# Performance work log

Measured on AMD Instinct MI355X. Metric: run time of the kernel, lower is better.

The kernel has to match this reference:

```python
import jax, jax.numpy as jnp
import numpy as np

BLOCK = 7          # hardcoded block_size
NUM_HEADS = 32     # CLIP RN50 attnpool heads
OUT_DIM = 512      # attnpool output dim == text feature dim
VOTE_CH = 512      # hardcoded channel count of `result`
NUM_BUCKETS = 6
_BOUNDS = jnp.array([8, 15, 22, 29, 36])  # class-index -> bucket boundaries from the if/elif chain


def _forward(image_features, text_features, pos_embed, q_w, q_b, k_w, k_b, v_w, v_b, out_w, out_b):
    B, C, Hf, Wf = image_features.shape
    Ho, Wo = Hf - BLOCK + 1, Wf - BLOCK + 1
    dt = image_features.dtype
    # --- batched extraction of all 7x7 sliding windows (replaces the i,j Python loop) ---
    ii = jnp.arange(Ho)[:, None] + jnp.arange(BLOCK)   # [Ho,7]
    jj = jnp.arange(Wo)[:, None] + jnp.arange(BLOCK)   # [Wo,7]
    rows = image_features[:, :, ii, :]                 # [B,C,Ho,7,Wf]
    pat = rows[:, :, :, :, jj]                         # [B,C,Ho,7,Wo,7]
    # row-major (di,dj) token order matches x.flatten(2) in CLIP AttentionPool2d
    tokens = pat.transpose(0, 2, 4, 3, 5, 1).reshape(B, Ho * Wo, BLOCK * BLOCK, C)  # [B,P,49,C]
    # --- CLIP AttentionPool2d, batched over all windows ---
    x = jnp.concatenate([tokens.mean(axis=2, keepdims=True), tokens], axis=2) + pos_embed  # [B,P,50,C]
    P, T = x.shape[1], x.shape[2]
    hd = C // NUM_HEADS
    q = (x[:, :, :1] @ q_w.T + q_b).reshape(B, P, 1, NUM_HEADS, hd)   # query = mean token
    k = (x @ k_w.T + k_b).reshape(B, P, T, NUM_HEADS, hd)
    v = (x @ v_w.T + v_b).reshape(B, P, T, NUM_HEADS, hd)
    attn = jax.nn.softmax(jnp.einsum('bpqhd,bpkhd->bphqk', q, k) * (float(hd) ** -0.5), axis=-1)
    pooled = jnp.einsum('bphqk,bpkhd->bpqhd', attn, v).reshape(B, P, C) @ out_w.T + out_b  # [B,P,512]
    # F.normalize followed by an extra /= norm (idempotent, kept for faithfulness)
    f = pooled / jnp.maximum(jnp.linalg.norm(pooled, axis=-1, keepdims=True), 1e-12)
    f = f / jnp.linalg.norm(f, axis=-1, keepdims=True)
    txt = text_features / jnp.linalg.norm(text_features, axis=-1, keepdims=True)
    logits = 100.0 * (f @ txt.T)                        # softmax is monotone -> argmax(logits)==argmax(probs)
    idx = jnp.argmax(logits, axis=-1)                   # [B,P]
    bucket = jnp.searchsorted(_BOUNDS, idx, side='right')  # 6-way grouping per the if/elif chain
    onehot = jax.nn.one_hot(bucket, NUM_BUCKETS, dtype=dt).reshape(B, Ho, Wo, NUM_BUCKETS).transpose(0, 3, 1, 2)
    # vote scatter-add (+1 over each 7x7 window) == full cross-correlation with a ones kernel
    kern = jnp.ones((NUM_BUCKETS, 1, BLOCK, BLOCK), dt)
    votes = jax.lax.conv_general_dilated(onehot, kern, (1, 1), [(BLOCK - 1, BLOCK - 1)] * 2,
                                         dimension_numbers=('NCHW', 'OIHW', 'NCHW'),
                                         feature_group_count=NUM_BUCKETS)  # [B,6,Hf,Wf]
    max_idx = jnp.argmax(votes, axis=1).astype(dt)      # torch.max returns first max index; argmax matches
    # `result` is re-created inside the per-image loop, so only slot B-1 survives (faithful to original)
    result = jnp.zeros((B, VOTE_CH, Hf, Wf), dt).at[B - 1].set(
        jnp.broadcast_to(max_idx[B - 1][None], (VOTE_CH, Hf, Wf)))
    return result / jnp.maximum(jnp.linalg.norm(result, axis=1, keepdims=True), 1e-12)


def setup_inputs() -> dict:
    key = jax.random.key(0)
    ks = jax.random.split(key, 8)
    B, C, Hf, Wf, NT = 2, 2048, 24, 24, 45
    w = lambda k, s: jax.random.normal(k, s, jnp.float32) * 0.02
    return {
        'image_features': jax.random.normal(ks[0], (B, C, Hf, Wf), jnp.float32),
        'text_features': jax.random.normal(ks[1], (NT, OUT_DIM), jnp.float32),
        'pos_embed': w(ks[2], (BLOCK * BLOCK + 1, C)),
        'q_w': w(ks[3], (C, C)), 'q_b': jnp.zeros((C,), jnp.float32),
        'k_w': w(ks[4], (C, C)), 'k_b': jnp.zeros((C,), jnp.float32),
        'v_w': w(ks[5], (C, C)), 'v_b': jnp.zeros((C,), jnp.float32),
        'out_w': w(ks[6], (OUT_DIM, C)), 'out_b': jnp.zeros((OUT_DIM,), jnp.float32),
    }


def reference(image_features, text_features, pos_embed, q_w, q_b, k_w, k_b, v_w, v_b, out_w, out_b):
    return _forward(image_features, text_features, pos_embed, q_w, q_b, k_w, k_b, v_w, v_b, out_w, out_b)
```

## Files before the change

kernel.cpp:

```cpp
#include <hip/hip_runtime.h>
#include <math.h>

#define CDIM 2048
#define HF 24
#define WF 24
#define PIX 576
#define HO 18
#define WO 18
#define NP 324
#define NHEAD 32
#define HD 64
#define NTOK 50
#define NTXT 45
#define OUTD 512
#define NKV 626
#define HJ (NHEAD * NTXT)
#define NROWS 640

typedef __attribute__((ext_vector_type(8))) short short8;
typedef __attribute__((ext_vector_type(4))) float f32x4;
typedef __attribute__((address_space(1))) const void as1c_void;
typedef __attribute__((address_space(3))) void as3_void;

__device__ inline unsigned bf16rn(float x) {
    unsigned u = __float_as_uint(x);
    return (u + 0x7FFFu + ((u >> 16) & 1u)) >> 16;
}
__device__ inline float bf16tof(unsigned h) { return __uint_as_float(h << 16); }

__device__ inline size_t frag_off(int row, int k) {
    return (size_t)(((row >> 4) * 64 + (k >> 5)) * 512)
         + (size_t)(((k & 31) >> 3) * 128 + (row & 15) * 8 + (k & 7));
}

__global__ void split_w_k(const float* __restrict__ kw, const float* __restrict__ vw, const float* __restrict__ qw,
                          ushort* __restrict__ WhK, ushort* __restrict__ WlK,
                          ushort* __restrict__ WhV, ushort* __restrict__ WlV,
                          ushort* __restrict__ WhQ, ushort* __restrict__ WlQ) {
    int g = blockIdx.x * 256 + threadIdx.x;
    int sel = g >> 20;
    int off = (g & 1048575) * 4;
    const float* src = sel == 0 ? kw : sel == 1 ? vw : qw;
    ushort* dh = sel == 0 ? WhK : sel == 1 ? WhV : WhQ;
    ushort* dl = sel == 0 ? WlK : sel == 1 ? WlV : WlQ;
    float4 v = *(const float4*)(src + off);
    float xs[4] = {v.x, v.y, v.z, v.w};
    ushort h[4], l[4];
#pragma unroll
    for (int i = 0; i < 4; ++i) {
        unsigned hh = bf16rn(xs[i]);
        h[i] = (ushort)hh;
        l[i] = (ushort)bf16rn(xs[i] - bf16tof(hh));
    }
    int m = off >> 11, k0 = off & 2047;
    size_t fo = frag_off(m, k0);
    *(ushort4*)(dh + fo) = make_ushort4(h[0], h[1], h[2], h[3]);
    *(ushort4*)(dl + fo) = make_ushort4(l[0], l[1], l[2], l[3]);
}

__global__ __launch_bounds__(256) void split_xt_k(const float* __restrict__ feat1,
                                                  ushort* __restrict__ Xh, ushort* __restrict__ Xl) {
    __shared__ float tile[64][65];
    int n0 = blockIdx.x * 64, c0 = blockIdx.y * 64, tid = threadIdx.x;
#pragma unroll
    for (int i = 0; i < 16; ++i) {
        int idx = tid + i * 256;
        int cc = idx >> 6, nn = idx & 63;
        tile[cc][nn] = feat1[(size_t)(c0 + cc) * PIX + n0 + nn];
    }
    __syncthreads();
#pragma unroll
    for (int i = 0; i < 16; ++i) {
        int idx = tid + i * 256;
        int nn = idx >> 6, cc = idx & 63;
        float x = tile[cc][nn];
        unsigned hh = bf16rn(x);
        size_t fo = frag_off(n0 + nn, c0 + cc);
        Xh[fo] = (ushort)hh;
        Xl[fo] = (ushort)bf16rn(x - bf16tof(hh));
    }
}

__global__ void split_pos_k(const float* __restrict__ pos,
                            ushort* __restrict__ Xh, ushort* __restrict__ Xl) {
    int g = blockIdx.x * 256 + threadIdx.x;
    int r = g >> 9;
    int c = (g & 511) * 4;
    float4 v = make_float4(0.f, 0.f, 0.f, 0.f);
    if (r < 50) v = *(const float4*)(pos + (size_t)r * CDIM + c);
    float xs[4] = {v.x, v.y, v.z, v.w};
    ushort h[4], l[4];
#pragma unroll
    for (int i = 0; i < 4; ++i) {
        unsigned hh = bf16rn(xs[i]);
        h[i] = (ushort)hh;
        l[i] = (ushort)bf16rn(xs[i] - bf16tof(hh));
    }
    size_t fo = frag_off(576 + r, c);
    *(ushort4*)(Xh + fo) = make_ushort4(h[0], h[1], h[2], h[3]);
    *(ushort4*)(Xl + fo) = make_ushort4(l[0], l[1], l[2], l[3]);
}

#define BUFB 24576
__global__ __launch_bounds__(256, 2) void gemm_bf16_k(
    const ushort* __restrict__ WhK, const ushort* __restrict__ WlK,
    const ushort* __restrict__ WhV, const ushort* __restrict__ WlV,
    const ushort* __restrict__ WhQ, const ushort* __restrict__ WlQ,
    const ushort* __restrict__ Xh, const ushort* __restrict__ Xl,
    const float* __restrict__ k_b, const float* __restrict__ v_b, const float* __restrict__ q_b,
    float* __restrict__ Kbuf, float* __restrict__ Vbuf, float* __restrict__ Qfull)
{
    __shared__ char smem[3 * BUFB];
    int z = blockIdx.z;
    const ushort* Wh = z == 0 ? WhK : z == 1 ? WhV : WhQ;
    const ushort* Wl = z == 0 ? WlK : z == 1 ? WlV : WlQ;
    const float* bias = z == 0 ? k_b : z == 1 ? v_b : q_b;
    float* out = z == 0 ? Kbuf : z == 1 ? Vbuf : Qfull;
    int m0 = blockIdx.x * 128, n0 = blockIdx.y * 64;

    int tid = threadIdx.x, wid = tid >> 6, lane = tid & 63;
    int wm = wid >> 1, wn = wid & 1;

    const char* gsrc[6];
    int ldsoff[6];
#pragma unroll
    for (int i = 0; i < 6; ++i) {
        int g = wid * 6 + i;
        const ushort* src; int r16; int off;
        if (g < 8)       { src = Wh; r16 = (m0 >> 4) + g;        off = g * 1024; }
        else if (g < 16) { src = Wl; r16 = (m0 >> 4) + (g - 8);  off = 8192 + (g - 8) * 1024; }
        else if (g < 20) { src = Xh; r16 = (n0 >> 4) + (g - 16); off = 16384 + (g - 16) * 1024; }
        else             { src = Xl; r16 = (n0 >> 4) + (g - 20); off = 20480 + (g - 20) * 1024; }
        gsrc[i] = (const char*)src + ((size_t)r16 * 64 * 1024) + lane * 16;
        ldsoff[i] = off;
    }

    f32x4 acc[4][2];
#pragma unroll
    for (int a = 0; a < 4; ++a)
#pragma unroll
        for (int b = 0; b < 2; ++b) acc[a][b] = (f32x4)0.f;

#pragma unroll
    for (int i = 0; i < 6; ++i)
        __builtin_amdgcn_global_load_lds((as1c_void*)(gsrc[i]),
                                         (as3_void*)(smem + ldsoff[i]), 16, 0, 0);
#pragma unroll
    for (int i = 0; i < 6; ++i)
        __builtin_amdgcn_global_load_lds((as1c_void*)(gsrc[i] + 1024),
                                         (as3_void*)(smem + BUFB + ldsoff[i]), 16, 0, 0);
    asm volatile("s_waitcnt vmcnt(6)" ::: "memory");
    __builtin_amdgcn_s_barrier();
    asm volatile("" ::: "memory");

    for (int t = 0; t < 64; ++t) {
        char* rbuf = smem + (t % 3) * BUFB;
        if (t < 62) {
            char* wbuf = smem + ((t + 2) % 3) * BUFB;
#pragma unroll
            for (int i = 0; i < 6; ++i)
                __builtin_amdgcn_global_load_lds((as1c_void*)(gsrc[i] + (size_t)(t + 2) * 1024),
                                                 (as3_void*)(wbuf + ldsoff[i]), 16, 0, 0);
        }

        short8 ah[4], al[4];
#pragma unroll
        for (int fm = 0; fm < 4; ++fm) {
            int s = wm * 4 + fm;
            ah[fm] = *(const short8*)(rbuf + s * 1024 + lane * 16);
            al[fm] = *(const short8*)(rbuf + 8192 + s * 1024 + lane * 16);
        }
        short8 bh[2], bl[2];
#pragma unroll
        for (int fn = 0; fn < 2; ++fn) {
            int s = wn * 2 + fn;
            bh[fn] = *(const short8*)(rbuf + 16384 + s * 1024 + lane * 16);
            bl[fn] = *(const short8*)(rbuf + 20480 + s * 1024 + lane * 16);
        }
#pragma unroll
        for (int fn = 0; fn < 2; ++fn)
#pragma unroll
            for (int fm = 0; fm < 4; ++fm) {
                acc[fm][fn] = __builtin_amdgcn_mfma_f32_16x16x32_bf16(ah[fm], bh[fn], acc[fm][fn], 0, 0, 0);
                acc[fm][fn] = __builtin_amdgcn_mfma_f32_16x16x32_bf16(ah[fm], bl[fn], acc[fm][fn], 0, 0, 0);
                acc[fm][fn] = __builtin_amdgcn_mfma_f32_16x16x32_bf16(al[fm], bh[fn], acc[fm][fn], 0, 0, 0);
            }

        if (t < 62) asm volatile("s_waitcnt vmcnt(6)" ::: "memory");
        else        asm volatile("s_waitcnt vmcnt(0)" ::: "memory");
        __builtin_amdgcn_s_barrier();
        asm volatile("" ::: "memory");
    }

#pragma unroll
    for (int fm = 0; fm < 4; ++fm) {
        int mg = m0 + wm * 64 + fm * 16 + (lane >> 4) * 4;
        float4 bv = *(const float4*)(bias + mg);
#pragma unroll
        for (int fn = 0; fn < 2; ++fn) {
            int ng = n0 + wn * 32 + fn * 16 + (lane & 15);
            f32x4 o = acc[fm][fn];
            if (ng >= PIX) { o[0] += bv.x; o[1] += bv.y; o[2] += bv.z; o[3] += bv.w; }
            *(f32x4*)(out + (size_t)ng * CDIM + mg) = o;
        }
    }
}

__global__ __launch_bounds__(256) void qmean_k(const float* __restrict__ Qfull, float* __restrict__ Qm) {
    int p = blockIdx.x;
    int i = p / WO, j = p % WO;
    int c = blockIdx.y * 1024 + threadIdx.x * 4;
    float4 s = make_float4(0.f, 0.f, 0.f, 0.f);
#pragma unroll 7
    for (int t = 0; t < 49; ++t) {
        int px = (i + t / 7) * WF + (j + t % 7);
        float4 v = *(const float4*)(Qfull + (size_t)px * CDIM + c);
        s.x += v.x; s.y += v.y; s.z += v.z; s.w += v.w;
    }
    float4 p0 = *(const float4*)(Qfull + (size_t)PIX * CDIM + c);
    float4 r;
    r.x = s.x * (1.f / 49.f) + p0.x;
    r.y = s.y * (1.f / 49.f) + p0.y;
    r.z = s.z * (1.f / 49.f) + p0.z;
    r.w = s.w * (1.f / 49.f) + p0.w;
    *(float4*)(Qm + (size_t)p * CDIM + c) = r;
}

__global__ __launch_bounds__(256) void txtw_k(
    const float* __restrict__ txt, const float* __restrict__ out_w, const float* __restrict__ out_b,
    float* __restrict__ TW, float* __restrict__ cconst)
{
    __shared__ float ts[OUTD];
    __shared__ float red[256], redb[256];
    int j = blockIdx.x, cb = blockIdx.y, tid = threadIdx.x;

    float n2 = 0.f, db = 0.f;
    for (int o = tid; o < OUTD; o += 256) {
        float tv = txt[(size_t)j * OUTD + o];
        ts[o] = tv;
        n2 += tv * tv;
        db += tv * out_b[o];
    }
    red[tid] = n2; redb[tid] = db;
    __syncthreads();
    for (int s = 128; s > 0; s >>= 1) {
        if (tid < s) { red[tid] += red[tid + s]; redb[tid] += redb[tid + s]; }
        __syncthreads();
    }
    float inv = 1.f / sqrtf(red[0]);

    int c = cb * 256 + tid;
    float acc = 0.f;
    for (int o = 0; o < OUTD; ++o)
        acc += ts[o] * out_w[(size_t)o * CDIM + c];
    TW[(size_t)j * CDIM + c] = acc * inv;
    if (cb == 0 && tid == 0) cconst[j] = redb[0] * inv;
}

__global__ __launch_bounds__(256) void tv_k(
    const float* __restrict__ TW, const float* __restrict__ Vbuf, float* __restrict__ TV)
{
    __shared__ float TWs[NTXT * HD];
    __shared__ float Vs[8 * HD];
    int cg = blockIdx.x, h = blockIdx.y, tid = threadIdx.x;
    int c0 = cg * 8;

    for (int idx = tid; idx < NTXT * HD; idx += 256) {
        int j = idx / HD, d = idx % HD;
        TWs[idx] = TW[(size_t)j * CDIM + h * HD + d];
    }
    for (int idx = tid; idx < 8 * HD; idx += 256) {
        int c = idx / HD, d = idx % HD;
        int col = c0 + c;
        Vs[idx] = (col < NKV) ? Vbuf[(size_t)col * CDIM + h * HD + d] : 0.f;
    }
    __syncthreads();

    for (int o = tid; o < 8 * NTXT; o += 256) {
        int c = o / NTXT, j = o % NTXT;
        int col = c0 + c;
        if (col >= NKV) continue;
        float acc = 0.f;
#pragma unroll
        for (int d = 0; d < HD; d += 4) {
            float4 tw = *(const float4*)&TWs[j * HD + d];
            float4 vv = *(const float4*)&Vs[c * HD + d];
            acc += tw.x * vv.x + tw.y * vv.y + tw.z * vv.z + tw.w * vv.w;
        }
        TV[(size_t)col * HJ + h * NTXT + j] = acc;
    }
}

__global__ __launch_bounds__(384) void attn_fused_k(
    const float* __restrict__ Kbuf, const float* __restrict__ Qm,
    const float* __restrict__ TV, float* __restrict__ pooledHJ)
{
    __shared__ float qs[8 * HD];
    __shared__ float scf[8][NTOK];
    __shared__ float scp[8][NTOK];
    __shared__ int win[49];

    int p = blockIdx.x, s = blockIdx.y;
    int h0 = s * 8;
    int pi = p / WO, pj = p % WO;
    int tid = threadIdx.x;

    if (tid < 128)
        *(float4*)&qs[tid * 4] = *(const float4*)(Qm + (size_t)p * CDIM + h0 * HD + tid * 4);
    if (tid < 49)
        win[tid] = (pi + tid / 7) * WF + (pj + tid % 7);
    __syncthreads();

    int grp = tid >> 4, gl = tid & 15;
#pragma unroll 3
    for (int i = 0; i < 33; ++i) {
        int pair = grp * 33 + i;
        int h, tt, row;
        if (pair < 392) { h = pair / 49; tt = pair % 49; row = win[tt]; }
        else { int q = pair - 392; h = q / 50; tt = q % 50; row = PIX + tt; }
        float4 kv = *(const float4*)(Kbuf + (size_t)row * CDIM + (h0 + h) * HD + gl * 4);
        float4 qv = *(const float4*)&qs[h * HD + gl * 4];
        float d = kv.x * qv.x + kv.y * qv.y + kv.z * qv.z + kv.w * qv.w;
        d += __shfl_xor(d, 1);
        d += __shfl_xor(d, 2);
        d += __shfl_xor(d, 4);
        d += __shfl_xor(d, 8);
        if (gl == 0) {
            if (pair < 392) scf[h][tt + 1] = d;
            else            scp[h][tt] = d;
        }
    }
    __syncthreads();

    if (tid < 8) {
        int h = tid;
        float sF = 0.f;
        for (int t = 1; t < NTOK; ++t) sF += scf[h][t];
        scf[h][0] = sF * (1.f / 49.f);
        float m = -1e30f;
        for (int t = 0; t < NTOK; ++t) {
            float sc = (scf[h][t] + scp[h][t]) * 0.125f;
            scp[h][t] = sc;
            m = fmaxf(m, sc);
        }
        float ssum = 0.f;
        for (int t = 0; t < NTOK; ++t) { float e = expf(scp[h][t] - m); scf[h][t] = e; ssum += e; }
        float inv = 1.f / ssum;
        for (int t = 0; t < NTOK; ++t) scf[h][t] *= inv;
    }
    __syncthreads();

    if (tid < 360) {
        int o = s * 360 + tid;
        int hloc = tid / 45;
        const float* apr = &scf[hloc][0];
        float lacc = 0.f, macc = 0.f;
#pragma unroll 7
        for (int t = 1; t < NTOK; ++t) {
            float a = apr[t];
            float v1 = TV[(size_t)win[t - 1] * HJ + o];
            float v2 = TV[(size_t)(PIX + t) * HJ + o];
            lacc += a * (v1 + v2);
            macc += v1;
        }
        float a0 = apr[0];
        lacc += a0 * (macc * (1.f / 49.f) + TV[(size_t)PIX * HJ + o]);
        pooledHJ[(size_t)p * HJ + o] = lacc;
    }
}

__global__ __launch_bounds__(64) void finish_k(const float* __restrict__ pooledHJ,
                                               const float* __restrict__ cconst,
                                               int* __restrict__ bucket) {
    __shared__ float lg[NTXT];
    int p = blockIdx.x, lane = threadIdx.x;
    if (lane < NTXT) {
        float s = cconst[lane];
        const float* row = pooledHJ + (size_t)p * HJ;
#pragma unroll 8
        for (int h = 0; h < NHEAD; ++h) s += row[h * NTXT + lane];
        lg[lane] = s;
    }
    __syncthreads();
    if (lane == 0) {
        float best = lg[0]; int bi = 0;
        for (int j2 = 1; j2 < NTXT; ++j2)
            if (lg[j2] > best) { best = lg[j2]; bi = j2; }
        int bk = 0;
        const int bounds[5] = {8, 15, 22, 29, 36};
#pragma unroll
        for (int u = 0; u < 5; ++u) bk += (bi >= bounds[u]) ? 1 : 0;
        bucket[p] = bk;
    }
}

__global__ void votes_k(const int* __restrict__ bucket, float* __restrict__ maxval) {
    __shared__ int bk[NP];
    int tid = threadIdx.x;
    if (tid < NP) bk[tid] = bucket[tid];
    __syncthreads();
    if (tid < PIX) {
        int y = tid / WF, x = tid % WF;
        int cnt[6] = {0, 0, 0, 0, 0, 0};
        int i0 = (y - 6 < 0) ? 0 : y - 6;
        int i1 = (y > HO - 1) ? HO - 1 : y;
        int j0 = (x - 6 < 0) ? 0 : x - 6;
        int j1 = (x > WO - 1) ? WO - 1 : x;
        for (int i = i0; i <= i1; ++i)
            for (int j = j0; j <= j1; ++j)
                cnt[bk[i * WO + j]]++;
        int best = cnt[0], bi = 0;
#pragma unroll
        for (int ch = 1; ch < 6; ++ch)
            if (cnt[ch] > best) { best = cnt[ch]; bi = ch; }
        maxval[tid] = (bi > 0) ? 0.044194173824159216f : 0.f;
    }
}

__global__ void fill_k(const float* __restrict__ maxval, float* __restrict__ out) {
    int idx = blockIdx.x * 256 + threadIdx.x;
    const int HALF = OUTD * PIX;
    if (idx >= 2 * HALF) return;
    out[idx] = (idx < HALF) ? 0.f : maxval[idx % PIX];
}

extern "C" void kernel_launch(void* const* d_in, const int* in_sizes, int n_in,
                              void* d_out, int out_size, void* d_ws, size_t ws_size,
                              hipStream_t stream) {
    const float* imgf = (const float*)d_in[0];
    const float* txt  = (const float*)d_in[1];
    const float* pos  = (const float*)d_in[2];
    const float* q_w  = (const float*)d_in[3];
    const float* q_b  = (const float*)d_in[4];
    const float* k_w  = (const float*)d_in[5];
    const float* k_b  = (const float*)d_in[6];
    const float* v_w  = (const float*)d_in[7];
    const float* v_b  = (const float*)d_in[8];
    const float* o_w  = (const float*)d_in[9];
    const float* o_b  = (const float*)d_in[10];

    const float* feat1 = imgf + (size_t)1 * CDIM * PIX;

    float* ws = (float*)d_ws;
    float* Kbuf  = ws;
    float* Vbuf  = Kbuf + (size_t)NROWS * CDIM;
    float* Qfull = Vbuf + (size_t)NROWS * CDIM;
    float* Qm    = Qfull + (size_t)NROWS * CDIM;
    float* TW    = Qm + (size_t)NP * CDIM;
    float* cconst = TW + (size_t)NTXT * CDIM;
    float* TV    = cconst + 64;
    float* pooledHJ = TV + (size_t)NKV * HJ;
    int*   bucket = (int*)(pooledHJ + (size_t)NP * HJ);
    float* maxval = (float*)(bucket + NP);
    size_t foff = (size_t)(maxval + 576 - ws);
    foff = (foff + 3) & ~(size_t)3;
    ushort* WhK = (ushort*)(ws + foff);
    ushort* WlK = WhK + (size_t)CDIM * CDIM;
    ushort* WhV = WlK + (size_t)CDIM * CDIM;
    ushort* WlV = WhV + (size_t)CDIM * CDIM;
    ushort* WhQ = WlV + (size_t)CDIM * CDIM;
    ushort* WlQ = WhQ + (size_t)CDIM * CDIM;
    ushort* Xh  = WlQ + (size_t)CDIM * CDIM;
    ushort* Xl  = Xh + (size_t)NROWS * CDIM;

    split_w_k<<<dim3(12288), dim3(256), 0, stream>>>(k_w, v_w, q_w, WhK, WlK, WhV, WlV, WhQ, WlQ);
    split_xt_k<<<dim3(9, 32), dim3(256), 0, stream>>>(feat1, Xh, Xl);
    split_pos_k<<<dim3(128), dim3(256), 0, stream>>>(pos, Xh, Xl);
    gemm_bf16_k<<<dim3(16, 10, 3), dim3(256), 0, stream>>>(WhK, WlK, WhV, WlV, WhQ, WlQ,
                                                           Xh, Xl, k_b, v_b, q_b, Kbuf, Vbuf, Qfull);
    qmean_k<<<dim3(NP, 2), dim3(256), 0, stream>>>(Qfull, Qm);
    txtw_k<<<dim3(NTXT, 8), dim3(256), 0, stream>>>(txt, o_w, o_b, TW, cconst);
    tv_k<<<dim3(79, 32), dim3(256), 0, stream>>>(TW, Vbuf, TV);
    attn_fused_k<<<dim3(NP, 4), dim3(384), 0, stream>>>(Kbuf, Qm, TV, pooledHJ);
    finish_k<<<dim3(NP), dim3(64), 0, stream>>>(pooledHJ, cconst, bucket);
    votes_k<<<dim3(1), dim3(576), 0, stream>>>(bucket, maxval);
    fill_k<<<dim3(2304), dim3(256), 0, stream>>>(maxval, (float*)d_out);
}
```

Before: 234.9 us.

## Precompute pos-embedding key scores in separate kernel and parallelize attention softmax

Moves the query·positional-key dot products into a new poss_k kernel that writes a per-window score table, which attn_fused_k then loads instead of computing them. The fused kernel's loop over key pairs shrinks to the 392 window tokens, and the per-head softmax is spread across 16 lanes per head with shuffle reductions instead of 8 serial threads. The grid is also flattened and remapped so neighbouring blocks cover adjacent windows and head groups, which may improve cache reuse. The cost is an extra kernel launch and an extra global buffer round trip.

```diff
diff --git a/kernel.cpp b/kernel.cpp
--- a/kernel.cpp
+++ b/kernel.cpp
@@ -226,6 +226,27 @@
     *(float4*)(Qm + (size_t)p * CDIM + c) = r;
 }
 
+__global__ __launch_bounds__(256) void poss_k(const float* __restrict__ Kbuf,
+                                              const float* __restrict__ Qm,
+                                              float* __restrict__ POSS) {
+    __shared__ float qsl[4 * HD];
+    int pb = blockIdx.x * 4, h = blockIdx.y, tid = threadIdx.x;
+    qsl[tid] = Qm[(size_t)(pb + (tid >> 6)) * CDIM + h * HD + (tid & 63)];
+    __syncthreads();
+    if (tid < 200) {
+        int pp = tid / 50, t = tid % 50;
+        const float* kp = Kbuf + (size_t)(PIX + t) * CDIM + h * HD;
+        const float* q = &qsl[pp * HD];
+        float dot = 0.f;
+#pragma unroll
+        for (int d = 0; d < HD; d += 4) {
+            float4 kv = *(const float4*)&kp[d];
+            dot += kv.x * q[d] + kv.y * q[d + 1] + kv.z * q[d + 2] + kv.w * q[d + 3];
+        }
+        POSS[(size_t)(pb + pp) * (NHEAD * NTOK) + h * NTOK + t] = dot;
+    }
+}
+
 __global__ __launch_bounds__(256) void txtw_k(
     const float* __restrict__ txt, const float* __restrict__ out_w, const float* __restrict__ out_b,
     float* __restrict__ TW, float* __restrict__ cconst)
@@ -293,14 +314,17 @@
 
 __global__ __launch_bounds__(384) void attn_fused_k(
     const float* __restrict__ Kbuf, const float* __restrict__ Qm,
-    const float* __restrict__ TV, float* __restrict__ pooledHJ)
+    const float* __restrict__ TV, const float* __restrict__ POSS,
+    float* __restrict__ pooledHJ)
 {
     __shared__ float qs[8 * HD];
     __shared__ float scf[8][NTOK];
     __shared__ float scp[8][NTOK];
     __shared__ int win[49];
 
-    int p = blockIdx.x, s = blockIdx.y;
+    int flat = blockIdx.x;
+    int s = (flat & 7) >> 1;
+    int p = (flat >> 3) * 2 + (flat & 1);
     int h0 = s * 8;
     int pi = p / WO, pj = p % WO;
     int tid = threadIdx.x;
@@ -309,44 +333,68 @@
         *(float4*)&qs[tid * 4] = *(const float4*)(Qm + (size_t)p * CDIM + h0 * HD + tid * 4);
     if (tid < 49)
         win[tid] = (pi + tid / 7) * WF + (pj + tid % 7);
+    for (int u = tid; u < 8 * NTOK; u += 384)
+        scp[u / NTOK][u % NTOK] = POSS[(size_t)p * (NHEAD * NTOK) + h0 * NTOK + u];
     __syncthreads();
 
     int grp = tid >> 4, gl = tid & 15;
-#pragma unroll 3
-    for (int i = 0; i < 33; ++i) {
-        int pair = grp * 33 + i;
-        int h, tt, row;
-        if (pair < 392) { h = pair / 49; tt = pair % 49; row = win[tt]; }
-        else { int q = pair - 392; h = q / 50; tt = q % 50; row = PIX + tt; }
-        float4 kv = *(const float4*)(Kbuf + (size_t)row * CDIM + (h0 + h) * HD + gl * 4);
-        float4 qv = *(const float4*)&qs[h * HD + gl * 4];
-        float d = kv.x * qv.x + kv.y * qv.y + kv.z * qv.z + kv.w * qv.w;
-        d += __shfl_xor(d, 1);
-        d += __shfl_xor(d, 2);
-        d += __shfl_xor(d, 4);
-        d += __shfl_xor(d, 8);
-        if (gl == 0) {
-            if (pair < 392) scf[h][tt + 1] = d;
-            else            scp[h][tt] = d;
-        }
-    }
-    __syncthreads();
-
-    if (tid < 8) {
-        int h = tid;
-        float sF = 0.f;
-        for (int t = 1; t < NTOK; ++t) sF += scf[h][t];
-        scf[h][0] = sF * (1.f / 49.f);
-        float m = -1e30f;
-        for (int t = 0; t < NTOK; ++t) {
-            float sc = (scf[h][t] + scp[h][t]) * 0.125f;
-            scp[h][t] = sc;
-            m = fmaxf(m, sc);
-        }
-        float ssum = 0.f;
-        for (int t = 0; t < NTOK; ++t) { float e = expf(scp[h][t] - m); scf[h][t] = e; ssum += e; }
-        float inv = 1.f / ssum;
-        for (int t = 0; t < NTOK; ++t) scf[h][t] *= inv;
+    for (int i = 0; i < 17; ++i) {
+        int pair = i * 24 + grp;
+        if (pair < 392) {
+            int h = pair / 49, tt = pair % 49;
+            float4 kv = *(const float4*)(Kbuf + (size_t)win[tt] * CDIM + (h0 + h) * HD + gl * 4);
+            float4 qv = *(const float4*)&qs[h * HD + gl * 4];
+            float d = kv.x * qv.x + kv.y * qv.y + kv.z * qv.z + kv.w * qv.w;
+            d += __shfl_xor(d, 1);
+            d += __shfl_xor(d, 2);
+            d += __shfl_xor(d, 4);
+            d += __shfl_xor(d, 8);
+            if (gl == 0) scf[h][tt + 1] = d;
+        }
+    }
+    __syncthreads();
+
+    if (tid < 128) {
+        int h = grp;
+        float sloc = 0.f;
+#pragma unroll
+        for (int i = 0; i < 4; ++i) {
+            int t = gl + 16 * i;
+            if (t >= 1 && t < NTOK) sloc += scf[h][t];
+        }
+        sloc += __shfl_xor(sloc, 1); sloc += __shfl_xor(sloc, 2);
+        sloc += __shfl_xor(sloc, 4); sloc += __shfl_xor(sloc, 8);
+        float s0 = sloc * (1.f / 49.f);
+
+        float sc[4];
+        float mloc = -1e30f;
+#pragma unroll
+        for (int i = 0; i < 4; ++i) {
+            int t = gl + 16 * i;
+            if (t < NTOK) {
+                float base = (t == 0) ? s0 : scf[h][t];
+                sc[i] = (base + scp[h][t]) * 0.125f;
+                mloc = fmaxf(mloc, sc[i]);
+            }
+        }
+        mloc = fmaxf(mloc, __shfl_xor(mloc, 1)); mloc = fmaxf(mloc, __shfl_xor(mloc, 2));
+        mloc = fmaxf(mloc, __shfl_xor(mloc, 4)); mloc = fmaxf(mloc, __shfl_xor(mloc, 8));
+
+        float ev[4];
+        float eloc = 0.f;
+#pragma unroll
+        for (int i = 0; i < 4; ++i) {
+            int t = gl + 16 * i;
+            if (t < NTOK) { ev[i] = expf(sc[i] - mloc); eloc += ev[i]; }
+        }
+        eloc += __shfl_xor(eloc, 1); eloc += __shfl_xor(eloc, 2);
+        eloc += __shfl_xor(eloc, 4); eloc += __shfl_xor(eloc, 8);
+        float inv = 1.f / eloc;
+#pragma unroll
+        for (int i = 0; i < 4; ++i) {
+            int t = gl + 16 * i;
+            if (t < NTOK) scf[h][t] = ev[i] * inv;
+        }
     }
     __syncthreads();
 
@@ -450,7 +498,8 @@
     float* cconst = TW + (size_t)NTXT * CDIM;
     float* TV    = cconst + 64;
     float* pooledHJ = TV + (size_t)NKV * HJ;
-    int*   bucket = (int*)(pooledHJ + (size_t)NP * HJ);
+    float* POSS  = pooledHJ + (size_t)NP * HJ;
+    int*   bucket = (int*)(POSS + (size_t)NP * NHEAD * NTOK);
     float* maxval = (float*)(bucket + NP);
     size_t foff = (size_t)(maxval + 576 - ws);
     foff = (foff + 3) & ~(size_t)3;
@@ -469,9 +518,10 @@
     gemm_bf16_k<<<dim3(16, 10, 3), dim3(256), 0, stream>>>(WhK, WlK, WhV, WlV, WhQ, WlQ,
                                                            Xh, Xl, k_b, v_b, q_b, Kbuf, Vbuf, Qfull);
     qmean_k<<<dim3(NP, 2), dim3(256), 0, stream>>>(Qfull, Qm);
+    poss_k<<<dim3(81, 32), dim3(256), 0, stream>>>(Kbuf, Qm, POSS);
     txtw_k<<<dim3(NTXT, 8), dim3(256), 0, stream>>>(txt, o_w, o_b, TW, cconst);
     tv_k<<<dim3(79, 32), dim3(256), 0, stream>>>(TW, Vbuf, TV);
-    attn_fused_k<<<dim3(NP, 4), dim3(384), 0, stream>>>(Kbuf, Qm, TV, pooledHJ);
+    attn_fused_k<<<dim3(NP * 4), dim3(384), 0, stream>>>(Kbuf, Qm, TV, POSS, pooledHJ);
     finish_k<<<dim3(NP), dim3(64), 0, stream>>>(pooledHJ, cconst, bucket);
     votes_k<<<dim3(1), dim3(576), 0, stream>>>(bucket, maxval);
     fill_k<<<dim3(2304), dim3(256), 0, stream>>>(maxval, (float*)d_out);
```

New measurement: 228.4 us. 2.7% less time.
